# Kernel tuning notes

Measured on AMD Instinct MI355X. Metric: run time of the kernel, lower is better.

## Reference

```python
import jax, jax.numpy as jnp
import numpy as np

B, S, T, E, H, VIN, VOUT = 64, 64, 32, 512, 1024, 32000, 32000


def setup_inputs() -> dict:
    key = jax.random.key(0)
    ks = jax.random.split(key, 12)
    rn = lambda k, shape, s=0.02: jax.random.normal(k, shape, jnp.float32) * s
    return {
        "src": jax.random.randint(ks[0], (B, S), 0, VIN),
        "tgt": jax.random.randint(ks[1], (B, T), 0, VOUT),
        "enc_emb": rn(ks[2], (VIN, E)),
        "dec_emb": rn(ks[3], (VOUT, E)),
        "enc_Wih": rn(ks[4], (4 * H, E)),
        "enc_Whh": rn(ks[5], (4 * H, H)),
        "enc_bih": jnp.zeros((4 * H,), jnp.float32),
        "enc_bhh": jnp.zeros((4 * H,), jnp.float32),
        "dec_Wih": rn(ks[6], (4 * H, E + H)),
        "dec_Whh": rn(ks[7], (4 * H, H)),
        "dec_bih": jnp.zeros((4 * H,), jnp.float32),
        "dec_bhh": jnp.zeros((4 * H,), jnp.float32),
        "attn_W": rn(ks[8], (H, 2 * H)),
        "attn_b": jnp.zeros((H,), jnp.float32),
        "v": jax.random.uniform(ks[9], (H,), jnp.float32),
        "fc_W": rn(ks[10], (VOUT, 2 * H)),
        "fc_b": jnp.zeros((VOUT,), jnp.float32),
    }


def _lstm_cell(x, h, c, Wih, Whh, bih, bhh):
    # torch gate order: i, f, g, o
    gates = x @ Wih.T + bih + h @ Whh.T + bhh
    i, f, g, o = jnp.split(gates, 4, axis=-1)
    c_new = jax.nn.sigmoid(f) * c + jax.nn.sigmoid(i) * jnp.tanh(g)
    h_new = jax.nn.sigmoid(o) * jnp.tanh(c_new)
    return h_new, c_new


def _forward(src, tgt, enc_emb, dec_emb, enc_Wih, enc_Whh, enc_bih, enc_bhh,
             dec_Wih, dec_Whh, dec_bih, dec_bhh, attn_W, attn_b, v, fc_W, fc_b):
    b, s = src.shape
    t_len = tgt.shape[1]
    hdim = enc_Whh.shape[1]

    # ---- encoder (single-layer LSTM, batch_first) ----
    x = enc_emb[src]  # [B,S,E] (dropout=0 in eval)

    def enc_step(carry, x_t):
        h, c = carry
        h, c = _lstm_cell(x_t, h, c, enc_Wih, enc_Whh, enc_bih, enc_bhh)
        return (h, c), h

    h0 = jnp.zeros((b, hdim), x.dtype)
    (h_f, c_f), enc_out_tm = jax.lax.scan(enc_step, (h0, h0), jnp.swapaxes(x, 0, 1))
    enc_out = jnp.swapaxes(enc_out_tm, 0, 1)  # [B,S,H]

    # hidden.detach() in torch
    h_f = jax.lax.stop_gradient(h_f)
    c_f = jax.lax.stop_gradient(c_f)

    # split attn_W for the concat(hidden, enc_out) linear
    Wh, We = attn_W[:, :hdim], attn_W[:, hdim:]
    enc_proj = jnp.einsum('bsh,kh->bsk', enc_out, We)  # hoisted, [B,S,H]

    def dec_step(carry, tok):
        h, c = carry
        emb = dec_emb[tok]  # [B,E]
        # Bahdanau attention: tanh(Linear(cat(h, enc_out))) . v
        energy = jnp.tanh(h @ Wh.T[None] if False else jnp.tanh((h @ Wh.T)[:, None, :] + enc_proj + attn_b))
        energy = jnp.tanh((h @ Wh.T)[:, None, :] + enc_proj + attn_b)  # [B,S,H]
        scores = jnp.einsum('bsh,h->bs', energy, v)
        a = jax.nn.softmax(scores, axis=1)
        context = jnp.einsum('bs,bsh->bh', a, enc_out)  # [B,H]
        rnn_in = jnp.concatenate([emb, context], axis=-1)
        h_new, c_new = _lstm_cell(rnn_in, h, c, dec_Wih, dec_Whh, dec_bih, dec_bhh)
        logits = jnp.concatenate([h_new, context], axis=-1) @ fc_W.T + fc_b
        return (h_new, c_new), logits

    # teacher_forcing_ratio = 1.0 -> input at step t is tgt[:, t-1]
    toks_tm = jnp.swapaxes(tgt[:, : t_len - 1], 0, 1)  # [T-1, B]
    _, logits_tm = jax.lax.scan(dec_step, (h_f, c_f), toks_tm)  # [T-1,B,V]
    logits = jnp.swapaxes(logits_tm, 0, 1)  # [B,T-1,V]
    zeros0 = jnp.zeros((b, 1, fc_W.shape[0]), logits.dtype)
    return jnp.concatenate([zeros0, logits], axis=1)  # [B,T,V]


def reference(src, tgt, enc_emb, dec_emb, enc_Wih, enc_Whh, enc_bih, enc_bhh,
              dec_Wih, dec_Whh, dec_bih, dec_bhh, attn_W, attn_b, v, fc_W, fc_b):
    return _forward(src, tgt, enc_emb, dec_emb, enc_Wih, enc_Whh, enc_bih, enc_bhh,
                    dec_Wih, dec_Whh, dec_bih, dec_bhh, attn_W, attn_b, v, fc_W, fc_b)
```

## Files before the change

### kernel.cpp

```cpp
#include <hip/hip_runtime.h>
#include <hip/hip_bf16.h>

typedef __bf16 bf16x8 __attribute__((ext_vector_type(8)));
typedef float  f32x4  __attribute__((ext_vector_type(4)));
typedef _Float16 h16x8 __attribute__((ext_vector_type(8)));

__device__ __forceinline__ unsigned short f2b(float f) {
    union { float f; unsigned u; } w; w.f = f;
    unsigned u = w.u + 0x7FFF + ((w.u >> 16) & 1);
    return (unsigned short)(u >> 16);
}
__device__ __forceinline__ float tanhfast(float x) {
    float e = __expf(2.0f * x);
    return 1.0f - 2.0f / (e + 1.0f);
}

__device__ __forceinline__ void stU(unsigned* p, unsigned v) {
    __hip_atomic_store(p, v, __ATOMIC_RELAXED, __HIP_MEMORY_SCOPE_AGENT);
}
__device__ __forceinline__ void stS(unsigned short* p, unsigned short v) {
    __hip_atomic_store(p, v, __ATOMIC_RELAXED, __HIP_MEMORY_SCOPE_AGENT);
}
__device__ __forceinline__ void stF(float* p, float v) {
    __hip_atomic_store(p, v, __ATOMIC_RELAXED, __HIP_MEMORY_SCOPE_AGENT);
}
__device__ __forceinline__ int ldI(const int* p) {
    return __hip_atomic_load((int*)p, __ATOMIC_RELAXED, __HIP_MEMORY_SCOPE_AGENT);
}
__device__ __forceinline__ void stI(int* p, int v) {
    __hip_atomic_store(p, v, __ATOMIC_RELAXED, __HIP_MEMORY_SCOPE_AGENT);
}

#define GLD16(g, l) __builtin_amdgcn_global_load_lds( \
    (const __attribute__((address_space(1))) void*)(g), \
    (__attribute__((address_space(3))) void*)(l), 16, 0, 0)

#define SLOT_STRIDE 16
#define NPOLL 256

__device__ __forceinline__ void gbar(int* slots, int* gen, int target) {
    asm volatile("s_waitcnt vmcnt(0)" ::: "memory");
    __syncthreads();
    if (blockIdx.x == 0) {
        if (threadIdx.x == 0) stI(slots, target);
        if (threadIdx.x < NPOLL) {
            while (ldI(slots + threadIdx.x * SLOT_STRIDE) < target)
                __builtin_amdgcn_s_sleep(1);
        }
        __syncthreads();
        if (threadIdx.x == 0) stI(gen, target);
    } else {
        if (threadIdx.x == 0) {
            stI(slots + blockIdx.x * SLOT_STRIDE, target);
            while (ldI(gen) < target)
                __builtin_amdgcn_s_sleep(1);
        }
        __syncthreads();
    }
}

__device__ __forceinline__ void mac16L(const unsigned short* A, const bf16x8* BL,
                                       f32x4& acc) {
    bf16x8 a[16];
#pragma unroll
    for (int kk = 0; kk < 16; ++kk) a[kk] = *(const bf16x8*)(A + kk * 32);
#pragma unroll
    for (int kk = 0; kk < 16; ++kk)
        acc = __builtin_amdgcn_mfma_f32_16x16x32_bf16(a[kk], BL[kk * 64], acc, 0, 0, 0);
}
__device__ __forceinline__ void mac4L(const unsigned short* A, const bf16x8* BL,
                                      f32x4& acc) {
    bf16x8 a[4];
#pragma unroll
    for (int kk = 0; kk < 4; ++kk) a[kk] = *(const bf16x8*)(A + kk * 32);
#pragma unroll
    for (int kk = 0; kk < 4; ++kk)
        acc = __builtin_amdgcn_mfma_f32_16x16x32_bf16(a[kk], BL[kk * 64], acc, 0, 0, 0);
}


__global__ void k_gather(const float* __restrict__ emb, const int* __restrict__ tok,
                         unsigned short* __restrict__ out, int L, int ldtok) {
    long total = (long)L * 64 * 128;
    for (long i = (long)blockIdx.x * blockDim.x + threadIdx.x; i < total;
         i += (long)gridDim.x * blockDim.x) {
        int  e4 = (int)(i & 127);
        long r  = i >> 7;
        int  t  = (int)(r >> 6), b = (int)(r & 63);
        int  tk = tok[b * ldtok + t];
        float4 v = *(const float4*)(emb + (long)tk * 512 + e4 * 4);
        ushort4 o; o.x = f2b(v.x); o.y = f2b(v.y); o.z = f2b(v.z); o.w = f2b(v.w);
        *(ushort4*)(out + r * 512 + e4 * 4) = o;
    }
}

__global__ void k_conv(const float* __restrict__ in, unsigned short* __restrict__ out,
                       long N_, int K_, int ldin, int col0, int ldout, int outcol0, int reorder) {
    long total = N_ * (K_ >> 2);
    int kq = K_ >> 2;
    for (long i = (long)blockIdx.x * blockDim.x + threadIdx.x; i < total;
         i += (long)gridDim.x * blockDim.x) {
        long n = i / kq;
        int  k4 = (int)(i - n * kq) * 4;
        long row = reorder ? (long)((n & 3) * 1024 + (n >> 2)) : n;
        float4 v = *(const float4*)(in + row * ldin + col0 + k4);
        ushort4 o; o.x = f2b(v.x); o.y = f2b(v.y); o.z = f2b(v.z); o.w = f2b(v.w);
        *(ushort4*)(out + n * ldout + outcol0 + k4) = o;
    }
}

__global__ void k_bias(const float* __restrict__ b1, const float* __restrict__ b2,
                       float* __restrict__ out) {
    int n = blockIdx.x * blockDim.x + threadIdx.x;
    if (n < 4096) {
        int row = (n & 3) * 1024 + (n >> 2);
        out[n] = b1[row] + b2[row];
    }
}

__global__ void k_zero0(float* __restrict__ out) {
    long total = 64L * 8000;
    for (long i = (long)blockIdx.x * blockDim.x + threadIdx.x; i < total;
         i += (long)gridDim.x * blockDim.x) {
        int b = (int)(i / 8000), q = (int)(i % 8000);
        float4 z = {0.f, 0.f, 0.f, 0.f};
        *(float4*)(out + (long)b * 1024000 + q * 4) = z;
    }
}

template<int BM, int BN, int WGM, int WGN, int FM, int FN>
__device__ __forceinline__ void gemm_core(
    const unsigned short* __restrict__ A, int lda,
    const unsigned short* __restrict__ B, int ldb,
    long m0, long n0, int K,
    unsigned short* As, unsigned short* Bs,
    f32x4 (&acc)[FM][FN])
{
    const int tid  = threadIdx.x;
    const int lane = tid & 63;
    const int wave = tid >> 6;
    const int wm = wave / WGN;
    const int wn = wave % WGN;
    const int srow = lane >> 2;
    const int scol = (lane & 3) * 8;
    const int frow = lane & 15;
    const int fcol = (lane >> 4) * 8;

    for (int k0 = 0; k0 < K; k0 += 32) {
        __syncthreads();
        for (int c = wave; c < BM / 16; c += 4) {
            const unsigned short* g = A + (m0 + c * 16 + srow) * (long)lda + k0 + scol;
            GLD16(g, As + c * 512);
        }
        for (int c = wave; c < BN / 16; c += 4) {
            const unsigned short* g = B + (n0 + c * 16 + srow) * (long)ldb + k0 + scol;
            GLD16(g, Bs + c * 512);
        }
        __syncthreads();
        bf16x8 af[FM], bfr[FN];
#pragma unroll
        for (int m = 0; m < FM; ++m)
            af[m] = *(const bf16x8*)(As + ((wm * FM + m) * 16 + frow) * 32 + fcol);
#pragma unroll
        for (int n = 0; n < FN; ++n)
            bfr[n] = *(const bf16x8*)(Bs + ((wn * FN + n) * 16 + frow) * 32 + fcol);
#pragma unroll
        for (int m = 0; m < FM; ++m)
#pragma unroll
            for (int n = 0; n < FN; ++n)
                acc[m][n] = __builtin_amdgcn_mfma_f32_16x16x32_bf16(af[m], bfr[n], acc[m][n], 0, 0, 0);
    }
}

template<int BM, int BN, int WGM, int WGN, int FM, int FN, int MODE>
__global__ __launch_bounds__(256) void k_gemm(
    const unsigned short* __restrict__ A, int lda,
    const unsigned short* __restrict__ B, int ldb,
    float* __restrict__ C, long ldc, const float* __restrict__ bias,
    int M, int N, int K, int Mreal)
{
    __shared__ __align__(16) unsigned short As[BM * 32];
    __shared__ __align__(16) unsigned short Bs[BN * 32];
    long m0, n0;
    if (MODE == 1) {
        int bid = blockIdx.x;
        int n = (bid & 7) * 32 + (bid >> 7);
        int m = (bid >> 3) & 15;
        if (n >= 250) return;
        m0 = (long)m * BM; n0 = (long)n * BN;
    } else {
        m0 = (long)blockIdx.y * BM; n0 = (long)blockIdx.x * BN;
    }
    f32x4 acc[FM][FN] = {};
    gemm_core<BM, BN, WGM, WGN, FM, FN>(A, lda, B, ldb, m0, n0, K, As, Bs, acc);

    const int lane = threadIdx.x & 63;
    const int wave = threadIdx.x >> 6;
    const int wm = wave / WGN, wn = wave % WGN;
#pragma unroll
    for (int n = 0; n < FN; ++n) {
        long col = n0 + wn * FN * 16 + n * 16 + (lane & 15);
        float bv = bias ? bias[col] : 0.0f;
#pragma unroll
        for (int m = 0; m < FM; ++m) {
            int rl = wm * FM * 16 + m * 16 + (lane >> 4) * 4;
#pragma unroll
            for (int q = 0; q < 4; ++q) {
                long r = m0 + rl + q;
                float val = acc[m][n][q] + bv;
                if (MODE == 0) {
                    C[r * ldc + col] = val;
                } else if (MODE == 2) {
                    ((_Float16*)C)[r * ldc + col] = (_Float16)val;
                } else {
                    if (r < Mreal) {
                        long orow = (r & 63) * 32 + (r >> 6) + 1;
                        C[orow * ldc + col] = val;
                    }
                }
            }
        }
    }
}

__global__ __launch_bounds__(512, 2) void k_enc(
    const unsigned short* __restrict__ W,
    const float* __restrict__ pre,
    unsigned short* __restrict__ hsl,
    unsigned short* __restrict__ enc_out,
    unsigned short* __restrict__ eoT,
    unsigned short* __restrict__ hS0,
    float* __restrict__ cspill,
    int* slots, int* gen)
{
    __shared__ __align__(16) unsigned short WL[16 * 1024];
    __shared__ float gs[64 * 16];
    const int blk = blockIdx.x, tid = threadIdx.x;
    const int lane = tid & 63, wave = tid >> 6;
    const int rt = wave >> 1, kh = wave & 1;
    const int n0 = blk * 16;
    const int grow = (rt * 16 + (lane >> 4) * 4) * 16 + (lane & 15);
    const int pb = tid >> 1, pjl = (tid & 1) * 2;
    const int jg = blk * 4 + pjl;
    for (int i = tid; i < 2048; i += 512) {
        int r = i & 15, k8 = i >> 4;
        ((bf16x8*)WL)[k8 * 16 + r] = *(const bf16x8*)(W + (long)(n0 + r) * 1024 + k8 * 8);
    }
    const bf16x8* BL = (const bf16x8*)WL + ((long)kh * 64 + (lane >> 4)) * 16 + (lane & 15);
    float c0 = 0.f, c1 = 0.f;
    float4 pr0 = {}, pr1 = {};
    if (tid < 128) {
        pr0 = *(const float4*)(pre + (long)pb * 4096 + n0 + pjl * 4);
        pr1 = *(const float4*)(pre + (long)pb * 4096 + n0 + pjl * 4 + 4);
    }
    __syncthreads();
    int bt = 0;
    for (int t = 0; t < 64; ++t) {
        const unsigned short* Ar = hsl + (long)t * 65536
            + (long)(rt * 16 + (lane & 15)) * 1024 + kh * 512 + (lane >> 4) * 8;
        f32x4 acc = {};
        mac16L(Ar, BL, acc);
        if (kh == 0) {
#pragma unroll
            for (int q = 0; q < 4; ++q) gs[grow + q * 16] = acc[q];
        }
        __syncthreads();
        if (kh == 1) {
#pragma unroll
            for (int q = 0; q < 4; ++q) atomicAdd(&gs[grow + q * 16], acc[q]);
        }
        __syncthreads();
        if (tid < 128) {
            float4 gA = *(const float4*)(gs + pb * 16 + pjl * 4);
            float4 gB = *(const float4*)(gs + pb * 16 + pjl * 4 + 4);
            float h0v, h1v;
            {
                float gi = gA.x + pr0.x, gf = gA.y + pr0.y, gg = gA.z + pr0.z, go = gA.w + pr0.w;
                float i_ = 1.f / (1.f + __expf(-gi)), f_ = 1.f / (1.f + __expf(-gf));
                float g_ = tanhfast(gg), o_ = 1.f / (1.f + __expf(-go));
                c0 = f_ * c0 + i_ * g_; h0v = o_ * tanhfast(c0);
            }
            {
                float gi = gB.x + pr1.x, gf = gB.y + pr1.y, gg = gB.z + pr1.z, go = gB.w + pr1.w;
                float i_ = 1.f / (1.f + __expf(-gi)), f_ = 1.f / (1.f + __expf(-gf));
                float g_ = tanhfast(gg), o_ = 1.f / (1.f + __expf(-go));
                c1 = f_ * c1 + i_ * g_; h1v = o_ * tanhfast(c1);
            }
            unsigned short hb0 = f2b(h0v), hb1 = f2b(h1v);
            unsigned pk = (unsigned)hb0 | ((unsigned)hb1 << 16);
            stU((unsigned*)(hsl + (long)(t + 1) * 65536 + (long)pb * 1024 + jg), pk);
            *(unsigned*)(enc_out + ((long)pb * 64 + t) * 1024 + jg) = pk;
            eoT[((long)pb * 1024 + jg) * 64 + t]     = hb0;
            eoT[((long)pb * 1024 + jg + 1) * 64 + t] = hb1;
            if (t < 63) {
                pr0 = *(const float4*)(pre + (long)(t + 1) * 262144 + (long)pb * 4096 + n0 + pjl * 4);
                pr1 = *(const float4*)(pre + (long)(t + 1) * 262144 + (long)pb * 4096 + n0 + pjl * 4 + 4);
            } else {
                *(unsigned*)(hS0 + (long)pb * 1024 + jg) = pk;
                cspill[(long)pb * 1024 + jg]     = c0;
                cspill[(long)pb * 1024 + jg + 1] = c1;
            }
        }
        gbar(slots, gen, ++bt);
    }
}

__global__ __launch_bounds__(512, 2) void k_dec(
    const unsigned short* __restrict__ Wh,
    const unsigned short* __restrict__ Wc,
    const float* __restrict__ pre,
    const _Float16* __restrict__ proj16,
    const unsigned short* __restrict__ eoT,
    const float* __restrict__ v,
    const float* __restrict__ cspill,
    unsigned short* __restrict__ hS,
    unsigned short* __restrict__ ctxS,
    float* __restrict__ qS,
    unsigned short* __restrict__ fcin,
    int* slots, int* gen)
{
    __shared__ __align__(16) unsigned short WcL[16 * 2048];
    __shared__ __align__(16) unsigned short WhL[16 * 1024];
    __shared__ float gs[64 * 16];
    __shared__ float qv[1024], vv[1024];
    __shared__ float sc[64], al[64];
    const int blk = blockIdx.x, tid = threadIdx.x;
    const int lane = tid & 63, wave = tid >> 6;
    const int rt = wave >> 1, kh = wave & 1;
    const int n0 = blk * 16;
    const int nq = blk >> 2, mt = blk & 3;
    const int grow = (rt * 16 + (lane >> 4) * 4) * 16 + (lane & 15);
    const int pb = tid >> 1, pjl = (tid & 1) * 2;
    const int jg = blk * 4 + pjl;
    for (int i = tid; i < 4096; i += 512) {
        int r = i & 15, k8 = i >> 4;
        ((bf16x8*)WcL)[k8 * 16 + r] = *(const bf16x8*)(Wc + (long)(n0 + r) * 2048 + k8 * 8);
    }
    for (int i = tid; i < 2048; i += 512) {
        int r = i & 15, k8 = i >> 4;
        ((bf16x8*)WhL)[k8 * 16 + r] = *(const bf16x8*)(Wh + (long)(nq * 16 + r) * 1024 + k8 * 8);
    }
    const bf16x8* BLc = (const bf16x8*)WcL + ((long)kh * 128 + (lane >> 4)) * 16 + (lane & 15);
    const bf16x8* BLq = (const bf16x8*)WhL + ((long)wave * 16 + (lane >> 4)) * 16 + (lane & 15);
    if (tid < 256) {
        float4 v4 = *(const float4*)(v + tid * 4);
        *(float4*)(vv + tid * 4) = v4;
    }
    float c0 = 0.f, c1 = 0.f;
    if (tid < 128) {
        c0 = cspill[(long)pb * 1024 + jg];
        c1 = cspill[(long)pb * 1024 + jg + 1];
    }
    __syncthreads();
    int bt = 0;
    for (int t = 0; t < 31; ++t) {
        const unsigned short* hSt   = hS   + (long)t * 65536;
        const unsigned short* ctxSt = ctxS + (long)t * 65536;
        float4 pr0 = {}, pr1 = {};
        if (tid < 128) {
            pr0 = *(const float4*)(pre + (long)t * 262144 + (long)pb * 4096 + n0 + pjl * 4);
            pr1 = *(const float4*)(pre + (long)t * 262144 + (long)pb * 4096 + n0 + pjl * 4 + 4);
        }
        {
            if (tid < 256) gs[tid] = 0.f;
            __syncthreads();
            const unsigned short* Ar = hSt + (long)(mt * 16 + (lane & 15)) * 1024
                                           + wave * 128 + (lane >> 4) * 8;
            f32x4 qa = {};
            mac4L(Ar, BLq, qa);
#pragma unroll
            for (int q = 0; q < 4; ++q)
                atomicAdd(&gs[((lane >> 4) * 4 + q) * 16 + (lane & 15)], qa[q]);
            __syncthreads();
            if (tid < 256)
                stF(qS + (long)t * 65536 + (long)(mt * 16 + (tid >> 4)) * 1024
                        + nq * 16 + (tid & 15), gs[tid]);
        }
        gbar(slots, gen, ++bt);
        if (blk < 64) {
            const int b = blk;
            if (tid < 256)
                *(float4*)(qv + tid * 4) =
                    *(const float4*)(qS + (long)t * 65536 + (long)b * 1024 + tid * 4);
            __syncthreads();
            int s = tid >> 3, part = tid & 7;
            const h16x8* pp = (const h16x8*)(proj16 + ((long)b * 64 + s) * 1024 + part * 128);
            float a_ = 0.f;
#pragma unroll 4
            for (int d = 0; d < 16; ++d) {
                h16x8 pv = pp[d];
                int h = part * 128 + d * 8;
#pragma unroll
                for (int j = 0; j < 8; ++j)
                    a_ += vv[h + j] * tanhfast(qv[h + j] + (float)pv[j]);
            }
            a_ += __shfl_xor(a_, 1);
            a_ += __shfl_xor(a_, 2);
            a_ += __shfl_xor(a_, 4);
            if (part == 0) sc[s] = a_;
            __syncthreads();
            if (tid < 64) {
                float x = sc[tid], mx = x;
                for (int o = 32; o; o >>= 1) mx = fmaxf(mx, __shfl_xor(mx, o));
                float e = __expf(x - mx), su = e;
                for (int o = 32; o; o >>= 1) su += __shfl_xor(su, o);
                al[tid] = e / su;
            }
            __syncthreads();
            int h0 = tid * 2;
            const bf16x8* ep = (const bf16x8*)(eoT + ((long)b * 1024 + h0) * 64);
            bf16x8 e[16];
#pragma unroll
            for (int c8 = 0; c8 < 16; ++c8) e[c8] = ep[c8];
            float cacc[2];
#pragma unroll
            for (int r = 0; r < 2; ++r) {
                float s_ = 0.f;
#pragma unroll
                for (int c8 = 0; c8 < 8; ++c8) {
                    bf16x8 v8 = e[r * 8 + c8];
#pragma unroll
                    for (int jj = 0; jj < 8; ++jj)
                        s_ += al[c8 * 8 + jj] * (float)v8[jj];
                }
                cacc[r] = s_;
            }
            unsigned pk0 = (unsigned)f2b(cacc[0]) | ((unsigned)f2b(cacc[1]) << 16);
            stU((unsigned*)(ctxS + (long)t * 65536 + (long)b * 1024 + h0), pk0);
            *(unsigned*)(fcin + ((long)t * 64 + b) * 2048 + 1024 + h0) = pk0;
        }
        gbar(slots, gen, ++bt);
        {
            const unsigned short* Asrc = (kh ? ctxSt : hSt)
                + (long)(rt * 16 + (lane & 15)) * 1024 + (lane >> 4) * 8;
            f32x4 acc = {};
            mac16L(Asrc,       BLc,        acc);
            mac16L(Asrc + 512, BLc + 1024, acc);
            if (kh == 0) {
#pragma unroll
                for (int q = 0; q < 4; ++q) gs[grow + q * 16] = acc[q];
            }
            __syncthreads();
            if (kh == 1) {
#pragma unroll
                for (int q = 0; q < 4; ++q) atomicAdd(&gs[grow + q * 16], acc[q]);
            }
            __syncthreads();
            if (tid < 128) {
                float4 gA = *(const float4*)(gs + pb * 16 + pjl * 4);
                float4 gB = *(const float4*)(gs + pb * 16 + pjl * 4 + 4);
                float h0v, h1v;
                {
                    float gi = gA.x + pr0.x, gf = gA.y + pr0.y, gg = gA.z + pr0.z, go = gA.w + pr0.w;
                    float i_ = 1.f / (1.f + __expf(-gi)), f_ = 1.f / (1.f + __expf(-gf));
                    float g_ = tanhfast(gg), o_ = 1.f / (1.f + __expf(-go));
                    c0 = f_ * c0 + i_ * g_; h0v = o_ * tanhfast(c0);
                }
                {
                    float gi = gB.x + pr1.x, gf = gB.y + pr1.y, gg = gB.z + pr1.z, go = gB.w + pr1.w;
                    float i_ = 1.f / (1.f + __expf(-gi)), f_ = 1.f / (1.f + __expf(-gf));
                    float g_ = tanhfast(gg), o_ = 1.f / (1.f + __expf(-go));
                    c1 = f_ * c1 + i_ * g_; h1v = o_ * tanhfast(c1);
                }
                unsigned pk = (unsigned)f2b(h0v) | ((unsigned)f2b(h1v) << 16);
                stU((unsigned*)(hS + (long)(t + 1) * 65536 + (long)pb * 1024 + jg), pk);
                *(unsigned*)(fcin + ((long)t * 64 + pb) * 2048 + jg) = pk;
            }
        }
        gbar(slots, gen, ++bt);
    }
}

extern "C" void kernel_launch(void* const* d_in, const int* in_sizes, int n_in,
                              void* d_out, int out_size, void* d_ws, size_t ws_size,
                              hipStream_t stream) {
    const int*   src     = (const int*)d_in[0];
    const int*   tgt     = (const int*)d_in[1];
    const float* enc_emb = (const float*)d_in[2];
    const float* dec_emb = (const float*)d_in[3];
    const float* enc_Wih = (const float*)d_in[4];
    const float* enc_Whh = (const float*)d_in[5];
    const float* enc_bih = (const float*)d_in[6];
    const float* enc_bhh = (const float*)d_in[7];
    const float* dec_Wih = (const float*)d_in[8];
    const float* dec_Whh = (const float*)d_in[9];
    const float* dec_bih = (const float*)d_in[10];
    const float* dec_bhh = (const float*)d_in[11];
    const float* attn_W  = (const float*)d_in[12];
    const float* attn_b  = (const float*)d_in[13];
    const float* vvec    = (const float*)d_in[14];
    const float* fc_W    = (const float*)d_in[15];
    const float* fc_b    = (const float*)d_in[16];
    float* out = (float*)d_out;

    char* ws = (char*)d_ws;
    size_t off = 0;
    auto alloc = [&](size_t bytes) -> char* {
        off = (off + 255) & ~(size_t)255;
        char* p = ws + off; off += bytes; return p;
    };
    unsigned short* wX      = (unsigned short*)alloc(4096UL * 512 * 2);
    unsigned short* weWih   = (unsigned short*)alloc(4096UL * 512 * 2);
    unsigned short* weWhh   = (unsigned short*)alloc(4096UL * 1024 * 2);
    float*          ebias   = (float*)alloc(4096UL * 4);
    float*          pre_enc = (float*)alloc(4096UL * 4096 * 4);
    unsigned short* enc_out = (unsigned short*)alloc(4096UL * 1024 * 2);
    unsigned short* eoT     = (unsigned short*)alloc(64UL * 1024 * 64 * 2);
    unsigned short* wWe     = (unsigned short*)alloc(1024UL * 1024 * 2);
    unsigned short* wWh     = (unsigned short*)alloc(1024UL * 1024 * 2);
    _Float16*       proj16  = (_Float16*)alloc(4096UL * 1024 * 2);
    float*          cbuf    = (float*)alloc(64UL * 1024 * 4);
    unsigned short* demb    = (unsigned short*)alloc(2048UL * 512 * 2);
    unsigned short* wDemb   = (unsigned short*)alloc(4096UL * 512 * 2);
    unsigned short* wCat    = (unsigned short*)alloc(4096UL * 2048 * 2);
    float*          dbias   = (float*)alloc(4096UL * 4);
    float*          pre_dec = (float*)alloc(2048UL * 4096 * 4);
    unsigned short* fcin    = (unsigned short*)alloc(2048UL * 2048 * 2);
    unsigned short* wFc     = (unsigned short*)alloc(32000UL * 2048 * 2);
    unsigned short* hslE    = (unsigned short*)alloc(65UL * 65536 * 2);
    unsigned short* hS      = (unsigned short*)alloc(32UL * 65536 * 2);
    unsigned short* ctxS    = (unsigned short*)alloc(32UL * 65536 * 2);
    float*          qS      = (float*)alloc(32UL * 65536 * 4);
    int*            bar     = (int*)alloc(65536);
    (void)ws_size; (void)in_sizes; (void)n_in; (void)out_size;

    int* slotsE = bar;
    int* genE   = bar + 4096;
    int* slotsD = bar + 8192;
    int* genD   = bar + 12288;

    hipMemsetAsync(bar, 0, 65536, stream);
    hipMemsetAsync(hslE, 0, 65536UL * 2, stream);
    k_zero0<<<512, 256, 0, stream>>>(out);

    k_gather<<<2048, 256, 0, stream>>>(enc_emb, src, wX, 64, 64);
    k_gather<<<1024, 256, 0, stream>>>(dec_emb, tgt, demb, 31, 32);
    k_conv<<<2048, 256, 0, stream>>>(enc_Wih, weWih, 4096, 512, 512, 0, 512, 0, 1);
    k_conv<<<2048, 256, 0, stream>>>(enc_Whh, weWhh, 4096, 1024, 1024, 0, 1024, 0, 1);
    k_conv<<<2048, 256, 0, stream>>>(dec_Wih, wDemb, 4096, 512, 1536, 0, 512, 0, 1);
    k_conv<<<2048, 256, 0, stream>>>(dec_Whh, wCat, 4096, 1024, 1024, 0, 2048, 0, 1);
    k_conv<<<2048, 256, 0, stream>>>(dec_Wih, wCat, 4096, 1024, 1536, 512, 2048, 1024, 1);
    k_conv<<<2048, 256, 0, stream>>>(attn_W, wWh, 1024, 1024, 2048, 0, 1024, 0, 0);
    k_conv<<<2048, 256, 0, stream>>>(attn_W, wWe, 1024, 1024, 2048, 1024, 1024, 0, 0);
    k_conv<<<4096, 256, 0, stream>>>(fc_W, wFc, 32000, 2048, 2048, 0, 2048, 0, 0);
    k_bias<<<16, 256, 0, stream>>>(enc_bih, enc_bhh, ebias);
    k_bias<<<16, 256, 0, stream>>>(dec_bih, dec_bhh, dbias);

    k_gemm<128,128,2,2,4,4,0><<<dim3(32, 32), 256, 0, stream>>>(
        wX, 512, weWih, 512, pre_enc, 4096, ebias, 4096, 4096, 512, 4096);
    k_gemm<128,128,2,2,4,4,0><<<dim3(32, 16), 256, 0, stream>>>(
        demb, 512, wDemb, 512, pre_dec, 4096, dbias, 2048, 4096, 512, 2048);

    k_enc<<<256, 512, 0, stream>>>(weWhh, pre_enc, hslE, enc_out, eoT,
                                   hS, cbuf, slotsE, genE);

    k_gemm<128,128,2,2,4,4,2><<<dim3(8, 32), 256, 0, stream>>>(
        enc_out, 1024, wWe, 1024, (float*)proj16, 1024, attn_b, 4096, 1024, 1024, 4096);

    k_dec<<<256, 512, 0, stream>>>(wWh, wCat, pre_dec, proj16, eoT, vvec, cbuf,
                                   hS, ctxS, qS, fcin, slotsD, genD);

    k_gemm<128,128,2,2,4,4,1><<<dim3(4096), 256, 0, stream>>>(
        fcin, 2048, wFc, 2048, out, 32000, fc_b, 2048, 32000, 2048, 1984);
}
```

Measured before the change: 2.324 ms.

## Fuse output FC projection into decoder kernel via warp-specialized producer/consumer waves

The persistent decoder kernel now splits each block's waves in two. Waves 0-3 run the recurrent decoder steps and synchronise among themselves with LDS-flag barriers instead of __syncthreads. Waves 4-7 compute the vocabulary FC projection for each finished time step, polling an LDS flag, so the large output GEMM overlaps with the serial recurrence and the separate GEMM launch goes away. The costs are that half the waves now do the recurrent work with doubled per-wave K loops, occupancy drops to one block per CU, and the FC GEMM reads operands straight from global memory without LDS tiling.

```diff
diff --git a/kernel.cpp b/kernel.cpp
--- a/kernel.cpp
+++ b/kernel.cpp
@@ -29,6 +29,12 @@
 }
 __device__ __forceinline__ void stI(int* p, int v) {
     __hip_atomic_store(p, v, __ATOMIC_RELAXED, __HIP_MEMORY_SCOPE_AGENT);
+}
+__device__ __forceinline__ void stL(int* p, int v) {
+    __hip_atomic_store(p, v, __ATOMIC_RELAXED, __HIP_MEMORY_SCOPE_WORKGROUP);
+}
+__device__ __forceinline__ int ldL(const int* p) {
+    return __hip_atomic_load((int*)p, __ATOMIC_RELAXED, __HIP_MEMORY_SCOPE_WORKGROUP);
 }
 
 #define GLD16(g, l) __builtin_amdgcn_global_load_lds( \
@@ -68,13 +74,13 @@
     for (int kk = 0; kk < 16; ++kk)
         acc = __builtin_amdgcn_mfma_f32_16x16x32_bf16(a[kk], BL[kk * 64], acc, 0, 0, 0);
 }
-__device__ __forceinline__ void mac4L(const unsigned short* A, const bf16x8* BL,
+__device__ __forceinline__ void mac8L(const unsigned short* A, const bf16x8* BL,
                                       f32x4& acc) {
-    bf16x8 a[4];
-#pragma unroll
-    for (int kk = 0; kk < 4; ++kk) a[kk] = *(const bf16x8*)(A + kk * 32);
-#pragma unroll
-    for (int kk = 0; kk < 4; ++kk)
+    bf16x8 a[8];
+#pragma unroll
+    for (int kk = 0; kk < 8; ++kk) a[kk] = *(const bf16x8*)(A + kk * 32);
+#pragma unroll
+    for (int kk = 0; kk < 8; ++kk)
         acc = __builtin_amdgcn_mfma_f32_16x16x32_bf16(a[kk], BL[kk * 64], acc, 0, 0, 0);
 }
 
@@ -181,16 +187,8 @@
 {
     __shared__ __align__(16) unsigned short As[BM * 32];
     __shared__ __align__(16) unsigned short Bs[BN * 32];
-    long m0, n0;
-    if (MODE == 1) {
-        int bid = blockIdx.x;
-        int n = (bid & 7) * 32 + (bid >> 7);
-        int m = (bid >> 3) & 15;
-        if (n >= 250) return;
-        m0 = (long)m * BM; n0 = (long)n * BN;
-    } else {
-        m0 = (long)blockIdx.y * BM; n0 = (long)blockIdx.x * BN;
-    }
+    long m0 = (long)blockIdx.y * BM;
+    long n0 = (long)blockIdx.x * BN;
     f32x4 acc[FM][FN] = {};
     gemm_core<BM, BN, WGM, WGN, FM, FN>(A, lda, B, ldb, m0, n0, K, As, Bs, acc);
 
@@ -210,13 +208,8 @@
                 float val = acc[m][n][q] + bv;
                 if (MODE == 0) {
                     C[r * ldc + col] = val;
-                } else if (MODE == 2) {
+                } else {
                     ((_Float16*)C)[r * ldc + col] = (_Float16)val;
-                } else {
-                    if (r < Mreal) {
-                        long orow = (r & 63) * 32 + (r >> 6) + 1;
-                        C[orow * ldc + col] = val;
-                    }
                 }
             }
         }
@@ -305,7 +298,7 @@
     }
 }
 
-__global__ __launch_bounds__(512, 2) void k_dec(
+__global__ __launch_bounds__(512, 1) void k_dec(
     const unsigned short* __restrict__ Wh,
     const unsigned short* __restrict__ Wc,
     const float* __restrict__ pre,
@@ -317,6 +310,9 @@
     unsigned short* __restrict__ ctxS,
     float* __restrict__ qS,
     unsigned short* __restrict__ fcin,
+    const unsigned short* __restrict__ wFc,
+    const float* __restrict__ fc_b,
+    float* __restrict__ out,
     int* slots, int* gen)
 {
     __shared__ __align__(16) unsigned short WcL[16 * 2048];
@@ -324,14 +320,13 @@
     __shared__ float gs[64 * 16];
     __shared__ float qv[1024], vv[1024];
     __shared__ float sc[64], al[64];
+    __shared__ int dfl[6];
     const int blk = blockIdx.x, tid = threadIdx.x;
     const int lane = tid & 63, wave = tid >> 6;
-    const int rt = wave >> 1, kh = wave & 1;
     const int n0 = blk * 16;
     const int nq = blk >> 2, mt = blk & 3;
-    const int grow = (rt * 16 + (lane >> 4) * 4) * 16 + (lane & 15);
-    const int pb = tid >> 1, pjl = (tid & 1) * 2;
-    const int jg = blk * 4 + pjl;
+
+    if (tid < 6) dfl[tid] = 0;
     for (int i = tid; i < 4096; i += 512) {
         int r = i & 15, k8 = i >> 4;
         ((bf16x8*)WcL)[k8 * 16 + r] = *(const bf16x8*)(Wc + (long)(n0 + r) * 2048 + k8 * 8);
@@ -340,134 +335,204 @@
         int r = i & 15, k8 = i >> 4;
         ((bf16x8*)WhL)[k8 * 16 + r] = *(const bf16x8*)(Wh + (long)(nq * 16 + r) * 1024 + k8 * 8);
     }
-    const bf16x8* BLc = (const bf16x8*)WcL + ((long)kh * 128 + (lane >> 4)) * 16 + (lane & 15);
-    const bf16x8* BLq = (const bf16x8*)WhL + ((long)wave * 16 + (lane >> 4)) * 16 + (lane & 15);
     if (tid < 256) {
         float4 v4 = *(const float4*)(v + tid * 4);
         *(float4*)(vv + tid * 4) = v4;
     }
-    float c0 = 0.f, c1 = 0.f;
-    if (tid < 128) {
-        c0 = cspill[(long)pb * 1024 + jg];
-        c1 = cspill[(long)pb * 1024 + jg + 1];
-    }
     __syncthreads();
-    int bt = 0;
-    for (int t = 0; t < 31; ++t) {
-        const unsigned short* hSt   = hS   + (long)t * 65536;
-        const unsigned short* ctxSt = ctxS + (long)t * 65536;
-        float4 pr0 = {}, pr1 = {};
+
+    if (wave < 4) {
+        const int pb = tid >> 1, pjl = (tid & 1) * 2;
+        const int jg = blk * 4 + pjl;
+        const int grow = (wave * 16 + (lane >> 4) * 4) * 16 + (lane & 15);
+        const bf16x8* BLc = (const bf16x8*)WcL + (lane >> 4) * 16 + (lane & 15);
+        const bf16x8* BLq = (const bf16x8*)WhL + ((long)wave * 32 + (lane >> 4)) * 16 + (lane & 15);
+        float c0 = 0.f, c1 = 0.f;
         if (tid < 128) {
-            pr0 = *(const float4*)(pre + (long)t * 262144 + (long)pb * 4096 + n0 + pjl * 4);
-            pr1 = *(const float4*)(pre + (long)t * 262144 + (long)pb * 4096 + n0 + pjl * 4 + 4);
-        }
-        {
-            if (tid < 256) gs[tid] = 0.f;
-            __syncthreads();
-            const unsigned short* Ar = hSt + (long)(mt * 16 + (lane & 15)) * 1024
-                                           + wave * 128 + (lane >> 4) * 8;
-            f32x4 qa = {};
-            mac4L(Ar, BLq, qa);
-#pragma unroll
-            for (int q = 0; q < 4; ++q)
-                atomicAdd(&gs[((lane >> 4) * 4 + q) * 16 + (lane & 15)], qa[q]);
-            __syncthreads();
-            if (tid < 256)
+            c0 = cspill[(long)pb * 1024 + jg];
+            c1 = cspill[(long)pb * 1024 + jg + 1];
+        }
+        int ep = 0, bt = 0;
+
+        auto dbar = [&](int e) {
+            asm volatile("s_waitcnt vmcnt(0) lgkmcnt(0)" ::: "memory");
+            if (lane == 0) stL(&dfl[wave], e);
+            while (ldL(&dfl[lane & 3]) < e) __builtin_amdgcn_s_sleep(1);
+        };
+        auto gbarD = [&](int target) {
+            dbar(++ep);
+            if (wave == 0) {
+                if (blk == 0) {
+                    if (lane == 0) stI(slots, target);
+#pragma unroll
+                    for (int g2 = 0; g2 < 4; ++g2)
+                        while (ldI(slots + (lane * 4 + g2) * SLOT_STRIDE) < target)
+                            __builtin_amdgcn_s_sleep(1);
+                    if (lane == 0) stI(gen, target);
+                } else {
+                    if (lane == 0) {
+                        stI(slots + blk * SLOT_STRIDE, target);
+                        while (ldI(gen) < target) __builtin_amdgcn_s_sleep(1);
+                    }
+                }
+                if (lane == 0) stL(&dfl[4], target);
+            }
+            while (ldL(&dfl[4]) < target) __builtin_amdgcn_s_sleep(1);
+        };
+
+        for (int t = 0; t < 31; ++t) {
+            const unsigned short* hSt   = hS   + (long)t * 65536;
+            const unsigned short* ctxSt = ctxS + (long)t * 65536;
+            float4 pr0 = {}, pr1 = {};
+            if (tid < 128) {
+                pr0 = *(const float4*)(pre + (long)t * 262144 + (long)pb * 4096 + n0 + pjl * 4);
+                pr1 = *(const float4*)(pre + (long)t * 262144 + (long)pb * 4096 + n0 + pjl * 4 + 4);
+            }
+            {
+                gs[tid] = 0.f;
+                dbar(++ep);
+                const unsigned short* Ar = hSt + (long)(mt * 16 + (lane & 15)) * 1024
+                                               + wave * 256 + (lane >> 4) * 8;
+                f32x4 qa = {};
+                mac8L(Ar, BLq, qa);
+#pragma unroll
+                for (int q = 0; q < 4; ++q)
+                    atomicAdd(&gs[((lane >> 4) * 4 + q) * 16 + (lane & 15)], qa[q]);
+                dbar(++ep);
                 stF(qS + (long)t * 65536 + (long)(mt * 16 + (tid >> 4)) * 1024
                         + nq * 16 + (tid & 15), gs[tid]);
-        }
-        gbar(slots, gen, ++bt);
-        if (blk < 64) {
-            const int b = blk;
-            if (tid < 256)
+            }
+            gbarD(++bt);
+            if (blk < 64) {
+                const int b = blk;
                 *(float4*)(qv + tid * 4) =
                     *(const float4*)(qS + (long)t * 65536 + (long)b * 1024 + tid * 4);
-            __syncthreads();
-            int s = tid >> 3, part = tid & 7;
-            const h16x8* pp = (const h16x8*)(proj16 + ((long)b * 64 + s) * 1024 + part * 128);
-            float a_ = 0.f;
+                dbar(++ep);
+                int s = tid >> 2, part = tid & 3;
+                const h16x8* pp = (const h16x8*)(proj16 + ((long)b * 64 + s) * 1024 + part * 256);
+                float a_ = 0.f;
 #pragma unroll 4
-            for (int d = 0; d < 16; ++d) {
-                h16x8 pv = pp[d];
-                int h = part * 128 + d * 8;
-#pragma unroll
-                for (int j = 0; j < 8; ++j)
-                    a_ += vv[h + j] * tanhfast(qv[h + j] + (float)pv[j]);
-            }
-            a_ += __shfl_xor(a_, 1);
-            a_ += __shfl_xor(a_, 2);
-            a_ += __shfl_xor(a_, 4);
-            if (part == 0) sc[s] = a_;
-            __syncthreads();
-            if (tid < 64) {
-                float x = sc[tid], mx = x;
-                for (int o = 32; o; o >>= 1) mx = fmaxf(mx, __shfl_xor(mx, o));
-                float e = __expf(x - mx), su = e;
-                for (int o = 32; o; o >>= 1) su += __shfl_xor(su, o);
-                al[tid] = e / su;
-            }
-            __syncthreads();
-            int h0 = tid * 2;
-            const bf16x8* ep = (const bf16x8*)(eoT + ((long)b * 1024 + h0) * 64);
-            bf16x8 e[16];
-#pragma unroll
-            for (int c8 = 0; c8 < 16; ++c8) e[c8] = ep[c8];
-            float cacc[2];
-#pragma unroll
-            for (int r = 0; r < 2; ++r) {
-                float s_ = 0.f;
-#pragma unroll
-                for (int c8 = 0; c8 < 8; ++c8) {
-                    bf16x8 v8 = e[r * 8 + c8];
-#pragma unroll
-                    for (int jj = 0; jj < 8; ++jj)
-                        s_ += al[c8 * 8 + jj] * (float)v8[jj];
-                }
-                cacc[r] = s_;
-            }
-            unsigned pk0 = (unsigned)f2b(cacc[0]) | ((unsigned)f2b(cacc[1]) << 16);
-            stU((unsigned*)(ctxS + (long)t * 65536 + (long)b * 1024 + h0), pk0);
-            *(unsigned*)(fcin + ((long)t * 64 + b) * 2048 + 1024 + h0) = pk0;
-        }
-        gbar(slots, gen, ++bt);
-        {
-            const unsigned short* Asrc = (kh ? ctxSt : hSt)
-                + (long)(rt * 16 + (lane & 15)) * 1024 + (lane >> 4) * 8;
-            f32x4 acc = {};
-            mac16L(Asrc,       BLc,        acc);
-            mac16L(Asrc + 512, BLc + 1024, acc);
-            if (kh == 0) {
+                for (int d = 0; d < 32; ++d) {
+                    h16x8 pv = pp[d];
+                    int h = part * 256 + d * 8;
+#pragma unroll
+                    for (int j = 0; j < 8; ++j)
+                        a_ += vv[h + j] * tanhfast(qv[h + j] + (float)pv[j]);
+                }
+                a_ += __shfl_xor(a_, 1);
+                a_ += __shfl_xor(a_, 2);
+                if (part == 0) sc[s] = a_;
+                dbar(++ep);
+                if (tid < 64) {
+                    float x = sc[tid], mx = x;
+                    for (int o = 32; o; o >>= 1) mx = fmaxf(mx, __shfl_xor(mx, o));
+                    float e = __expf(x - mx), su = e;
+                    for (int o = 32; o; o >>= 1) su += __shfl_xor(su, o);
+                    al[tid] = e / su;
+                }
+                dbar(++ep);
+                int h0 = tid * 4;
+                float cacc[4];
+#pragma unroll
+                for (int r = 0; r < 4; ++r) {
+                    const bf16x8* ep2 = (const bf16x8*)(eoT + ((long)b * 1024 + h0 + r) * 64);
+                    bf16x8 e8[8];
+#pragma unroll
+                    for (int c8 = 0; c8 < 8; ++c8) e8[c8] = ep2[c8];
+                    float s_ = 0.f;
+#pragma unroll
+                    for (int c8 = 0; c8 < 8; ++c8) {
+#pragma unroll
+                        for (int jj = 0; jj < 8; ++jj)
+                            s_ += al[c8 * 8 + jj] * (float)e8[c8][jj];
+                    }
+                    cacc[r] = s_;
+                }
+                unsigned pk0 = (unsigned)f2b(cacc[0]) | ((unsigned)f2b(cacc[1]) << 16);
+                unsigned pk1 = (unsigned)f2b(cacc[2]) | ((unsigned)f2b(cacc[3]) << 16);
+                stU((unsigned*)(ctxS + (long)t * 65536 + (long)b * 1024 + h0), pk0);
+                stU((unsigned*)(ctxS + (long)t * 65536 + (long)b * 1024 + h0 + 2), pk1);
+                stU((unsigned*)(fcin + ((long)t * 64 + b) * 2048 + 1024 + h0), pk0);
+                stU((unsigned*)(fcin + ((long)t * 64 + b) * 2048 + 1024 + h0 + 2), pk1);
+            }
+            gbarD(++bt);
+            {
+                const unsigned short* Ah = hSt   + (long)(wave * 16 + (lane & 15)) * 1024 + (lane >> 4) * 8;
+                const unsigned short* Ac = ctxSt + (long)(wave * 16 + (lane & 15)) * 1024 + (lane >> 4) * 8;
+                f32x4 acc = {};
+                mac16L(Ah,       BLc,        acc);
+                mac16L(Ah + 512, BLc + 1024, acc);
+                mac16L(Ac,       BLc + 2048, acc);
+                mac16L(Ac + 512, BLc + 3072, acc);
 #pragma unroll
                 for (int q = 0; q < 4; ++q) gs[grow + q * 16] = acc[q];
-            }
-            __syncthreads();
-            if (kh == 1) {
-#pragma unroll
-                for (int q = 0; q < 4; ++q) atomicAdd(&gs[grow + q * 16], acc[q]);
-            }
-            __syncthreads();
-            if (tid < 128) {
-                float4 gA = *(const float4*)(gs + pb * 16 + pjl * 4);
-                float4 gB = *(const float4*)(gs + pb * 16 + pjl * 4 + 4);
-                float h0v, h1v;
-                {
-                    float gi = gA.x + pr0.x, gf = gA.y + pr0.y, gg = gA.z + pr0.z, go = gA.w + pr0.w;
-                    float i_ = 1.f / (1.f + __expf(-gi)), f_ = 1.f / (1.f + __expf(-gf));
-                    float g_ = tanhfast(gg), o_ = 1.f / (1.f + __expf(-go));
-                    c0 = f_ * c0 + i_ * g_; h0v = o_ * tanhfast(c0);
-                }
-                {
-                    float gi = gB.x + pr1.x, gf = gB.y + pr1.y, gg = gB.z + pr1.z, go = gB.w + pr1.w;
-                    float i_ = 1.f / (1.f + __expf(-gi)), f_ = 1.f / (1.f + __expf(-gf));
-                    float g_ = tanhfast(gg), o_ = 1.f / (1.f + __expf(-go));
-                    c1 = f_ * c1 + i_ * g_; h1v = o_ * tanhfast(c1);
-                }
-                unsigned pk = (unsigned)f2b(h0v) | ((unsigned)f2b(h1v) << 16);
-                stU((unsigned*)(hS + (long)(t + 1) * 65536 + (long)pb * 1024 + jg), pk);
-                *(unsigned*)(fcin + ((long)t * 64 + pb) * 2048 + jg) = pk;
-            }
-        }
-        gbar(slots, gen, ++bt);
+                dbar(++ep);
+                if (tid < 128) {
+                    float4 gA = *(const float4*)(gs + pb * 16 + pjl * 4);
+                    float4 gB = *(const float4*)(gs + pb * 16 + pjl * 4 + 4);
+                    float h0v, h1v;
+                    {
+                        float gi = gA.x + pr0.x, gf = gA.y + pr0.y, gg = gA.z + pr0.z, go = gA.w + pr0.w;
+                        float i_ = 1.f / (1.f + __expf(-gi)), f_ = 1.f / (1.f + __expf(-gf));
+                        float g_ = tanhfast(gg), o_ = 1.f / (1.f + __expf(-go));
+                        c0 = f_ * c0 + i_ * g_; h0v = o_ * tanhfast(c0);
+                    }
+                    {
+                        float gi = gB.x + pr1.x, gf = gB.y + pr1.y, gg = gB.z + pr1.z, go = gB.w + pr1.w;
+                        float i_ = 1.f / (1.f + __expf(-gi)), f_ = 1.f / (1.f + __expf(-gf));
+                        float g_ = tanhfast(gg), o_ = 1.f / (1.f + __expf(-go));
+                        c1 = f_ * c1 + i_ * g_; h1v = o_ * tanhfast(c1);
+                    }
+                    unsigned pk = (unsigned)f2b(h0v) | ((unsigned)f2b(h1v) << 16);
+                    stU((unsigned*)(hS + (long)(t + 1) * 65536 + (long)pb * 1024 + jg), pk);
+                    stU((unsigned*)(fcin + ((long)t * 64 + pb) * 2048 + jg), pk);
+                }
+            }
+            gbarD(++bt);
+            if (wave == 0 && lane == 0) stL(&dfl[5], t + 1);
+        }
+    } else {
+        int strip = blk * 4 + (wave - 4);
+        if (strip < 1000) {
+            const long bc = (long)strip * 32;
+            const int fr = lane & 15, fk = (lane >> 4) * 8;
+            float bv0 = fc_b[bc + fr], bv1 = fc_b[bc + 16 + fr];
+            for (int m2 = 0; m2 < 31; ++m2) {
+                while (ldL(&dfl[5]) < m2 + 1) __builtin_amdgcn_s_sleep(16);
+                f32x4 acc[4][2] = {};
+                const unsigned short* Ab = fcin + ((long)m2 * 64 + fr) * 2048 + fk;
+                const unsigned short* Bb = wFc + (bc + fr) * 2048 + fk;
+#pragma unroll 2
+                for (int k0 = 0; k0 < 2048; k0 += 32) {
+                    bf16x8 av[4], bvv[2];
+#pragma unroll
+                    for (int r = 0; r < 4; ++r)
+                        av[r] = *(const bf16x8*)(Ab + (long)r * 16 * 2048 + k0);
+#pragma unroll
+                    for (int c2 = 0; c2 < 2; ++c2)
+                        bvv[c2] = *(const bf16x8*)(Bb + (long)c2 * 16 * 2048 + k0);
+#pragma unroll
+                    for (int r = 0; r < 4; ++r)
+#pragma unroll
+                        for (int c2 = 0; c2 < 2; ++c2)
+                            acc[r][c2] = __builtin_amdgcn_mfma_f32_16x16x32_bf16(
+                                av[r], bvv[c2], acc[r][c2], 0, 0, 0);
+                }
+#pragma unroll
+                for (int c2 = 0; c2 < 2; ++c2) {
+                    long col = bc + c2 * 16 + fr;
+                    float bvs = c2 ? bv1 : bv0;
+#pragma unroll
+                    for (int r = 0; r < 4; ++r)
+#pragma unroll
+                        for (int q = 0; q < 4; ++q) {
+                            int rr = m2 * 64 + r * 16 + (lane >> 4) * 4 + q;
+                            long orow = (long)(rr & 63) * 32 + m2 + 1;
+                            out[orow * 32000 + col] = acc[r][c2][q] + bvs;
+                        }
+                }
+            }
+        }
     }
 }
 
@@ -558,8 +623,6 @@
         enc_out, 1024, wWe, 1024, (float*)proj16, 1024, attn_b, 4096, 1024, 1024, 4096);
 
     k_dec<<<256, 512, 0, stream>>>(wWh, wCat, pre_dec, proj16, eoT, vvec, cbuf,
-                                   hS, ctxS, qS, fcin, slotsD, genD);
-
-    k_gemm<128,128,2,2,4,4,1><<<dim3(4096), 256, 0, stream>>>(
-        fcin, 2048, wFc, 2048, out, 32000, fc_b, 2048, 32000, 2048, 1984);
-}
+                                   hS, ctxS, qS, fcin, wFc, fc_b, out,
+                                   slotsD, genD);
+}
```

Measured after the change: 2.867 ms. 1.23x slower.
